# Performance work log

Hardware: AMD Instinct MI355X
Metric: run time of the kernel (lower is better)

The kernel has to match this reference:

```python
import jax, jax.numpy as jnp
import numpy as np

B, NI, H, NC = 524288, 32, 128, 64


def _masks(ni, h):
    deg_in = jnp.arange(ni)                     # input layer: arange % ni == arange
    deg_hid = jnp.arange(h) % (ni - 1)
    deg_out = jnp.arange(2 * ni) % ni - 1
    m1 = (deg_hid[:, None] >= deg_in[None, :]).astype(jnp.float32)   # [H, NI]
    m2 = (deg_hid[:, None] >= deg_hid[None, :]).astype(jnp.float32)  # [H, H]
    m3 = (deg_out[:, None] >= deg_hid[None, :]).astype(jnp.float32)  # [2NI, H]
    return m1, m2, m3


def setup_inputs() -> dict:
    key = jax.random.key(0)
    ks = jax.random.split(key, 9)
    s = 0.05
    return {
        "x": jax.random.normal(ks[0], (B, NI), jnp.float32),
        "cond": jax.random.normal(ks[1], (B, NC), jnp.float32),
        "W1": jax.random.normal(ks[2], (H, NI), jnp.float32) * s,
        "b1": jnp.zeros((H,), jnp.float32),
        "Wc": jax.random.normal(ks[3], (H, NC), jnp.float32) * s,
        "W2": jax.random.normal(ks[4], (H, H), jnp.float32) * s,
        "b2": jnp.zeros((H,), jnp.float32),
        "W3": jax.random.normal(ks[5], (2 * NI, H), jnp.float32) * s,
        "b3": jnp.zeros((2 * NI,), jnp.float32),
    }


def reference(x, cond, W1, b1, Wc, W2, b2, W3, b3):
    ni = x.shape[1]
    h_dim = W1.shape[0]
    m1, m2, m3 = _masks(ni, h_dim)
    # joiner: masked linear + conditioning linear (no bias on cond)
    h = x @ (W1 * m1).T + b1 + cond @ Wc.T            # [B, H]
    h = jax.nn.relu(h)
    h = jax.nn.relu(h @ (W2 * m2).T + b2)             # [B, H]
    o = h @ (W3 * m3).T + b3                          # [B, 2NI]
    m_, a = o[:, :ni], o[:, ni:]
    a = jnp.clip(a, -5.0, 5.0)
    u = (x - m_) * jnp.exp(-a)
    logdet = -jnp.sum(a, axis=-1, keepdims=True)
    return u, logdet
```

## Files before the change

### kernel.cpp

```cpp
#include <hip/hip_runtime.h>


#define B_ROWS 524288
#define NI 32
#define HD 128
#define NC 64

#define L2_BASE 24
#define L3_BASE 56
#define N_FRAGS 72

typedef _Float16 half8 __attribute__((ext_vector_type(8)));
typedef float f32x4 __attribute__((ext_vector_type(4)));

__device__ inline f32x4 relu4(f32x4 v) {
  v[0] = fmaxf(v[0], 0.f); v[1] = fmaxf(v[1], 0.f);
  v[2] = fmaxf(v[2], 0.f); v[3] = fmaxf(v[3], 0.f);
  return v;
}

__device__ inline half8 cvt8(f32x4 lo, f32x4 hi) {
  half8 h;
  h[0] = (_Float16)lo[0]; h[1] = (_Float16)lo[1];
  h[2] = (_Float16)lo[2]; h[3] = (_Float16)lo[3];
  h[4] = (_Float16)hi[0]; h[5] = (_Float16)hi[1];
  h[6] = (_Float16)hi[2]; h[7] = (_Float16)hi[3];
  return h;
}

__global__ void prep_weights(const float* __restrict__ W1, const float* __restrict__ Wc,
                             const float* __restrict__ W2, const float* __restrict__ W3,
                             _Float16* __restrict__ wf) {
  int tid = blockIdx.x * blockDim.x + threadIdx.x;
  if (tid >= N_FRAGS * 64) return;
  int frag = tid >> 6;
  int lane = tid & 63;
  int q = lane >> 4, c = lane & 15;
  int L, jt, kt;
  if (frag < L2_BASE)      { L = 0; jt = frag / 3;              kt = frag % 3; }
  else if (frag < L3_BASE) { L = 1; jt = (frag - L2_BASE) >> 2; kt = (frag - L2_BASE) & 3; }
  else                     { L = 2; jt = (frag - L3_BASE) >> 2; kt = (frag - L3_BASE) & 3; }
  int j = jt * 16 + c;
  half8 v;
#pragma unroll
  for (int e = 0; e < 8; ++e) {
    int k = kt * 32 + (e >> 2) * 16 + q * 4 + (e & 3);
    float w;
    if (L == 0) {
      if (k < NI) w = ((j % 31) >= k) ? W1[j * NI + k] : 0.f;
      else        w = Wc[j * NC + (k - NI)];
    } else if (L == 1) {
      w = ((j % 31) >= (k % 31)) ? W2[j * HD + k] : 0.f;
    } else {
      w = (((j % 32) - 1) >= (k % 31)) ? W3[j * HD + k] : 0.f;
    }
    v[e] = (_Float16)w;
  }
  *(half8*)(wf + (size_t)tid * 8) = v;
}

__global__ __launch_bounds__(512, 4) void made_fused(
    const float* __restrict__ x, const float* __restrict__ cond,
    const float* __restrict__ b1, const float* __restrict__ b2,
    const float* __restrict__ b3, const _Float16* __restrict__ wf,
    float* __restrict__ out) {
  __shared__ __align__(16) _Float16 wlds[48 * 512];

  const int tid  = threadIdx.x;
  const int lane = tid & 63;
  const int wid  = tid >> 6;
  const int q = lane >> 4, c = lane & 15;
  const long rowbase = ((long)blockIdx.x * 8 + wid) * 32;

  {
    const char* gsrc = (const char*)(wf + L2_BASE * 512) + wid * 6144;
    char* lbase = (char*)wlds + wid * 6144;
#pragma unroll
    for (int i = 0; i < 6; ++i) {
      __builtin_amdgcn_global_load_lds(
          (const __attribute__((address_space(1))) void*)(gsrc + i * 1024 + lane * 16),
          (__attribute__((address_space(3))) void*)(lbase + i * 1024),
          16, 0, 0);
    }
  }

  half8 bf[3][2];
#pragma unroll
  for (int nt = 0; nt < 2; ++nt) {
    const float* xr = x    + (rowbase + nt * 16 + c) * NI;
    const float* cr = cond + (rowbase + nt * 16 + c) * NC;
    bf[0][nt] = cvt8(*(const f32x4*)(xr + q * 4), *(const f32x4*)(xr + 16 + q * 4));
    bf[1][nt] = cvt8(*(const f32x4*)(cr + q * 4), *(const f32x4*)(cr + 16 + q * 4));
    bf[2][nt] = cvt8(*(const f32x4*)(cr + 32 + q * 4), *(const f32x4*)(cr + 48 + q * 4));
  }

  f32x4 acc[4][2];
  half8 h1[4][2];
#pragma unroll
  for (int jh = 0; jh < 2; ++jh) {
#pragma unroll
    for (int j4 = 0; j4 < 4; ++j4) {
      f32x4 bv = *(const f32x4*)(b1 + (jh * 4 + j4) * 16 + q * 4);
      acc[j4][0] = bv; acc[j4][1] = bv;
    }
#pragma unroll
    for (int j4 = 0; j4 < 4; ++j4) {
      int jt = jh * 4 + j4;
#pragma unroll
      for (int kt = 0; kt < 3; ++kt) {
        half8 a = *(const half8*)(wf + (((jt * 3 + kt) * 64 + lane) << 3));
#pragma unroll
        for (int nt = 0; nt < 2; ++nt)
          acc[j4][nt] = __builtin_amdgcn_mfma_f32_16x16x32_f16(a, bf[kt][nt], acc[j4][nt], 0, 0, 0);
      }
    }
#pragma unroll
    for (int p = 0; p < 2; ++p)
#pragma unroll
      for (int nt = 0; nt < 2; ++nt)
        h1[jh * 2 + p][nt] = cvt8(relu4(acc[p * 2][nt]), relu4(acc[p * 2 + 1][nt]));
  }

  __syncthreads();

  half8 h2[4][2];
#pragma unroll
  for (int jh = 0; jh < 2; ++jh) {
#pragma unroll
    for (int j4 = 0; j4 < 4; ++j4) {
      f32x4 bv = *(const f32x4*)(b2 + (jh * 4 + j4) * 16 + q * 4);
      acc[j4][0] = bv; acc[j4][1] = bv;
    }
#pragma unroll
    for (int j4 = 0; j4 < 4; ++j4) {
      int jt = jh * 4 + j4;
#pragma unroll
      for (int kt = 0; kt < 4; ++kt) {
        half8 a = *(const half8*)(wlds + (((jt * 4 + kt) * 64 + lane) << 3));
#pragma unroll
        for (int nt = 0; nt < 2; ++nt)
          acc[j4][nt] = __builtin_amdgcn_mfma_f32_16x16x32_f16(a, h1[kt][nt], acc[j4][nt], 0, 0, 0);
      }
    }
#pragma unroll
    for (int p = 0; p < 2; ++p)
#pragma unroll
      for (int nt = 0; nt < 2; ++nt)
        h2[jh * 2 + p][nt] = cvt8(relu4(acc[p * 2][nt]), relu4(acc[p * 2 + 1][nt]));
  }

#pragma unroll
  for (int jt = 0; jt < 4; ++jt) {
    f32x4 bv = *(const f32x4*)(b3 + jt * 16 + q * 4);
    acc[jt][0] = bv; acc[jt][1] = bv;
  }
#pragma unroll
  for (int jt = 0; jt < 4; ++jt)
#pragma unroll
    for (int kt = 0; kt < 4; ++kt) {
      half8 a = *(const half8*)(wlds + (((32 + jt * 4 + kt) * 64 + lane) << 3));
#pragma unroll
      for (int nt = 0; nt < 2; ++nt)
        acc[jt][nt] = __builtin_amdgcn_mfma_f32_16x16x32_f16(a, h2[kt][nt], acc[jt][nt], 0, 0, 0);
    }

#pragma unroll
  for (int nt = 0; nt < 2; ++nt) {
    long m = rowbase + nt * 16 + c;
    const float* xr = x + m * NI;
    f32x4 xa = *(const f32x4*)(xr + q * 4);
    f32x4 xb = *(const f32x4*)(xr + 16 + q * 4);
    f32x4 mva = acc[0][nt], mvb = acc[1][nt];
    f32x4 ava = acc[2][nt], avb = acc[3][nt];
    f32x4 ua, ub;
    float s = 0.f;
#pragma unroll
    for (int i = 0; i < 4; ++i) {
      float aa = fminf(fmaxf(ava[i], -5.f), 5.f);
      float ab = fminf(fmaxf(avb[i], -5.f), 5.f);
      ua[i] = (xa[i] - mva[i]) * __expf(-aa);
      ub[i] = (xb[i] - mvb[i]) * __expf(-ab);
      s += aa + ab;
    }
    *(f32x4*)(out + m * NI + q * 4) = ua;
    *(f32x4*)(out + m * NI + 16 + q * 4) = ub;
    s += __shfl_xor(s, 16);
    s += __shfl_xor(s, 32);
    if (q == 0) out[(long)B_ROWS * NI + m] = -s;
  }
}

extern "C" void kernel_launch(void* const* d_in, const int* in_sizes, int n_in,
                              void* d_out, int out_size, void* d_ws, size_t ws_size,
                              hipStream_t stream) {
  const float* x    = (const float*)d_in[0];
  const float* cond = (const float*)d_in[1];
  const float* W1   = (const float*)d_in[2];
  const float* b1   = (const float*)d_in[3];
  const float* Wc   = (const float*)d_in[4];
  const float* W2   = (const float*)d_in[5];
  const float* b2   = (const float*)d_in[6];
  const float* W3   = (const float*)d_in[7];
  const float* b3   = (const float*)d_in[8];
  _Float16* wf = (_Float16*)d_ws;

  prep_weights<<<(N_FRAGS * 64 + 255) / 256, 256, 0, stream>>>(W1, Wc, W2, W3, wf);
  made_fused<<<B_ROWS / 256, 512, 0, stream>>>(x, cond, b1, b2, b3, wf, (float*)d_out);
}
```

Before: 292.9 us.

## Make blocks persistent over row tiles with register double-buffered input prefetch

Each block now loops over four 128-row tiles, one 16-row tile per wave. The next tile's x and cond rows are prefetched into registers while the current tile runs its MFMAs. All three layers' weights and the biases are staged into LDS once per block, so the layer-1 weights are no longer read from global memory and the weight loads are spread over more rows. The trade-off is less MFMA work per wave per weight fetch (one 16-row N tile instead of two), more LDS, and fewer blocks in flight.

```diff
diff --git a/kernel.cpp b/kernel.cpp
--- a/kernel.cpp
+++ b/kernel.cpp
@@ -5,6 +5,7 @@
 #define NI 32
 #define HD 128
 #define NC 64
+#define ITERS 4
 
 #define L2_BASE 24
 #define L3_BASE 56
@@ -59,134 +60,139 @@
   *(half8*)(wf + (size_t)tid * 8) = v;
 }
 
+
+#define BODY(RX, RC, NRX, NRC, IT)                                            \
+  {                                                                           \
+    half8 bf0 = cvt8(RX[0], RX[1]);                                           \
+    half8 bf1 = cvt8(RC[0], RC[1]);                                           \
+    half8 bf2 = cvt8(RC[2], RC[3]);                                           \
+    if ((IT) < ITERS - 1) {     \
+      long nr = blockBase + ((IT) + 1) * 128 + wid * 16 + c;                  \
+      const f32x4* xr = (const f32x4*)(x + nr * NI);                          \
+      const f32x4* cr = (const f32x4*)(cond + nr * NC);                       \
+      NRX[0] = xr[q];     NRX[1] = xr[4 + q];                                 \
+      NRC[0] = cr[q];     NRC[1] = cr[4 + q];                                 \
+      NRC[2] = cr[8 + q]; NRC[3] = cr[12 + q];                                \
+    }                                                                         \
+    f32x4 acc[4]; half8 h1[4], h2[4];                                         \
+         \
+    _Pragma("unroll")                                                         \
+    for (int jh = 0; jh < 2; ++jh) {                                          \
+      _Pragma("unroll")                                                       \
+      for (int j4 = 0; j4 < 4; ++j4)                                          \
+        acc[j4] = *(const f32x4*)(blds + (jh * 4 + j4) * 16 + q * 4);         \
+      _Pragma("unroll")                                                       \
+      for (int j4 = 0; j4 < 4; ++j4) {                                        \
+        int jt = jh * 4 + j4;                                                 \
+        _Pragma("unroll")                                                     \
+        for (int kt = 0; kt < 3; ++kt) {                                      \
+          half8 a = *(const half8*)(wlds + (((jt * 3 + kt) * 64 + lane) << 3)); \
+          half8 bb = (kt == 0) ? bf0 : ((kt == 1) ? bf1 : bf2);               \
+          acc[j4] = __builtin_amdgcn_mfma_f32_16x16x32_f16(a, bb, acc[j4], 0, 0, 0); \
+        }                                                                     \
+      }                                                                       \
+      _Pragma("unroll")                                                       \
+      for (int p = 0; p < 2; ++p)                                             \
+        h1[jh * 2 + p] = cvt8(relu4(acc[p * 2]), relu4(acc[p * 2 + 1]));      \
+    }                                                                         \
+                                             \
+    _Pragma("unroll")                                                         \
+    for (int jh = 0; jh < 2; ++jh) {                                          \
+      _Pragma("unroll")                                                       \
+      for (int j4 = 0; j4 < 4; ++j4)                                          \
+        acc[j4] = *(const f32x4*)(blds + 128 + (jh * 4 + j4) * 16 + q * 4);   \
+      _Pragma("unroll")                                                       \
+      for (int j4 = 0; j4 < 4; ++j4) {                                        \
+        int jt = jh * 4 + j4;                                                 \
+        _Pragma("unroll")                                                     \
+        for (int kt = 0; kt < 4; ++kt) {                                      \
+          half8 a = *(const half8*)(wlds + (((L2_BASE + jt * 4 + kt) * 64 + lane) << 3)); \
+          acc[j4] = __builtin_amdgcn_mfma_f32_16x16x32_f16(a, h1[kt], acc[j4], 0, 0, 0); \
+        }                                                                     \
+      }                                                                       \
+      _Pragma("unroll")                                                       \
+      for (int p = 0; p < 2; ++p)                                             \
+        h2[jh * 2 + p] = cvt8(relu4(acc[p * 2]), relu4(acc[p * 2 + 1]));      \
+    }                                                                         \
+                \
+    _Pragma("unroll")                                                         \
+    for (int jt = 0; jt < 4; ++jt)                                            \
+      acc[jt] = *(const f32x4*)(blds + 256 + jt * 16 + q * 4);                \
+    _Pragma("unroll")                                                         \
+    for (int jt = 0; jt < 4; ++jt) {                                          \
+      _Pragma("unroll")                                                       \
+      for (int kt = 0; kt < 4; ++kt) {                                        \
+        half8 a = *(const half8*)(wlds + (((L3_BASE + jt * 4 + kt) * 64 + lane) << 3)); \
+        acc[jt] = __builtin_amdgcn_mfma_f32_16x16x32_f16(a, h2[kt], acc[jt], 0, 0, 0); \
+      }                                                                       \
+    }                                                                         \
+                      \
+    {                                                                         \
+      long m = blockBase + (IT) * 128 + wid * 16 + c;                         \
+      f32x4 xa = RX[0], xb = RX[1];                                           \
+      f32x4 ua, ub;                                                           \
+      float s = 0.f;                                                          \
+      _Pragma("unroll")                                                       \
+      for (int i = 0; i < 4; ++i) {                                           \
+        float aa = fminf(fmaxf(acc[2][i], -5.f), 5.f);                        \
+        float ab = fminf(fmaxf(acc[3][i], -5.f), 5.f);                        \
+        ua[i] = (xa[i] - acc[0][i]) * __expf(-aa);                            \
+        ub[i] = (xb[i] - acc[1][i]) * __expf(-ab);                            \
+        s += aa + ab;                                                         \
+      }                                                                       \
+      *(f32x4*)(out + m * NI + q * 4) = ua;                                   \
+      *(f32x4*)(out + m * NI + 16 + q * 4) = ub;                              \
+      s += __shfl_xor(s, 16);                                                 \
+      s += __shfl_xor(s, 32);                                                 \
+      if (q == 0) out[(long)B_ROWS * NI + m] = -s;                            \
+    }                                                                         \
+  }
+
 __global__ __launch_bounds__(512, 4) void made_fused(
     const float* __restrict__ x, const float* __restrict__ cond,
     const float* __restrict__ b1, const float* __restrict__ b2,
     const float* __restrict__ b3, const _Float16* __restrict__ wf,
     float* __restrict__ out) {
-  __shared__ __align__(16) _Float16 wlds[48 * 512];
+  __shared__ __align__(16) _Float16 wlds[N_FRAGS * 512];
+  __shared__ float blds[320];
 
   const int tid  = threadIdx.x;
   const int lane = tid & 63;
   const int wid  = tid >> 6;
   const int q = lane >> 4, c = lane & 15;
-  const long rowbase = ((long)blockIdx.x * 8 + wid) * 32;
+  const long blockBase = (long)blockIdx.x * (ITERS * 128);
 
   {
-    const char* gsrc = (const char*)(wf + L2_BASE * 512) + wid * 6144;
-    char* lbase = (char*)wlds + wid * 6144;
+    const char* gsrc = (const char*)wf + wid * 9216;
+    char* ldst = (char*)wlds + wid * 9216;
 #pragma unroll
-    for (int i = 0; i < 6; ++i) {
+    for (int i = 0; i < 9; ++i) {
       __builtin_amdgcn_global_load_lds(
           (const __attribute__((address_space(1))) void*)(gsrc + i * 1024 + lane * 16),
-          (__attribute__((address_space(3))) void*)(lbase + i * 1024),
+          (__attribute__((address_space(3))) void*)(ldst + i * 1024),
           16, 0, 0);
     }
   }
-
-  half8 bf[3][2];
-#pragma unroll
-  for (int nt = 0; nt < 2; ++nt) {
-    const float* xr = x    + (rowbase + nt * 16 + c) * NI;
-    const float* cr = cond + (rowbase + nt * 16 + c) * NC;
-    bf[0][nt] = cvt8(*(const f32x4*)(xr + q * 4), *(const f32x4*)(xr + 16 + q * 4));
-    bf[1][nt] = cvt8(*(const f32x4*)(cr + q * 4), *(const f32x4*)(cr + 16 + q * 4));
-    bf[2][nt] = cvt8(*(const f32x4*)(cr + 32 + q * 4), *(const f32x4*)(cr + 48 + q * 4));
-  }
-
-  f32x4 acc[4][2];
-  half8 h1[4][2];
-#pragma unroll
-  for (int jh = 0; jh < 2; ++jh) {
-#pragma unroll
-    for (int j4 = 0; j4 < 4; ++j4) {
-      f32x4 bv = *(const f32x4*)(b1 + (jh * 4 + j4) * 16 + q * 4);
-      acc[j4][0] = bv; acc[j4][1] = bv;
-    }
-#pragma unroll
-    for (int j4 = 0; j4 < 4; ++j4) {
-      int jt = jh * 4 + j4;
-#pragma unroll
-      for (int kt = 0; kt < 3; ++kt) {
-        half8 a = *(const half8*)(wf + (((jt * 3 + kt) * 64 + lane) << 3));
-#pragma unroll
-        for (int nt = 0; nt < 2; ++nt)
-          acc[j4][nt] = __builtin_amdgcn_mfma_f32_16x16x32_f16(a, bf[kt][nt], acc[j4][nt], 0, 0, 0);
-      }
-    }
-#pragma unroll
-    for (int p = 0; p < 2; ++p)
-#pragma unroll
-      for (int nt = 0; nt < 2; ++nt)
-        h1[jh * 2 + p][nt] = cvt8(relu4(acc[p * 2][nt]), relu4(acc[p * 2 + 1][nt]));
+  if (tid < 128)      blds[tid] = b1[tid];
+  else if (tid < 256) blds[tid] = b2[tid - 128];
+  else if (tid < 320) blds[tid] = b3[tid - 256];
+
+  f32x4 rxA[2], rcA[4], rxB[2], rcB[4];
+  {
+    long r = blockBase + wid * 16 + c;
+    const f32x4* xr = (const f32x4*)(x + r * NI);
+    const f32x4* cr = (const f32x4*)(cond + r * NC);
+    rxA[0] = xr[q];     rxA[1] = xr[4 + q];
+    rcA[0] = cr[q];     rcA[1] = cr[4 + q];
+    rcA[2] = cr[8 + q]; rcA[3] = cr[12 + q];
   }
 
   __syncthreads();
 
-  half8 h2[4][2];
-#pragma unroll
-  for (int jh = 0; jh < 2; ++jh) {
-#pragma unroll
-    for (int j4 = 0; j4 < 4; ++j4) {
-      f32x4 bv = *(const f32x4*)(b2 + (jh * 4 + j4) * 16 + q * 4);
-      acc[j4][0] = bv; acc[j4][1] = bv;
-    }
-#pragma unroll
-    for (int j4 = 0; j4 < 4; ++j4) {
-      int jt = jh * 4 + j4;
-#pragma unroll
-      for (int kt = 0; kt < 4; ++kt) {
-        half8 a = *(const half8*)(wlds + (((jt * 4 + kt) * 64 + lane) << 3));
-#pragma unroll
-        for (int nt = 0; nt < 2; ++nt)
-          acc[j4][nt] = __builtin_amdgcn_mfma_f32_16x16x32_f16(a, h1[kt][nt], acc[j4][nt], 0, 0, 0);
-      }
-    }
-#pragma unroll
-    for (int p = 0; p < 2; ++p)
-#pragma unroll
-      for (int nt = 0; nt < 2; ++nt)
-        h2[jh * 2 + p][nt] = cvt8(relu4(acc[p * 2][nt]), relu4(acc[p * 2 + 1][nt]));
-  }
-
-#pragma unroll
-  for (int jt = 0; jt < 4; ++jt) {
-    f32x4 bv = *(const f32x4*)(b3 + jt * 16 + q * 4);
-    acc[jt][0] = bv; acc[jt][1] = bv;
-  }
-#pragma unroll
-  for (int jt = 0; jt < 4; ++jt)
-#pragma unroll
-    for (int kt = 0; kt < 4; ++kt) {
-      half8 a = *(const half8*)(wlds + (((32 + jt * 4 + kt) * 64 + lane) << 3));
-#pragma unroll
-      for (int nt = 0; nt < 2; ++nt)
-        acc[jt][nt] = __builtin_amdgcn_mfma_f32_16x16x32_f16(a, h2[kt][nt], acc[jt][nt], 0, 0, 0);
-    }
-
-#pragma unroll
-  for (int nt = 0; nt < 2; ++nt) {
-    long m = rowbase + nt * 16 + c;
-    const float* xr = x + m * NI;
-    f32x4 xa = *(const f32x4*)(xr + q * 4);
-    f32x4 xb = *(const f32x4*)(xr + 16 + q * 4);
-    f32x4 mva = acc[0][nt], mvb = acc[1][nt];
-    f32x4 ava = acc[2][nt], avb = acc[3][nt];
-    f32x4 ua, ub;
-    float s = 0.f;
-#pragma unroll
-    for (int i = 0; i < 4; ++i) {
-      float aa = fminf(fmaxf(ava[i], -5.f), 5.f);
-      float ab = fminf(fmaxf(avb[i], -5.f), 5.f);
-      ua[i] = (xa[i] - mva[i]) * __expf(-aa);
-      ub[i] = (xb[i] - mvb[i]) * __expf(-ab);
-      s += aa + ab;
-    }
-    *(f32x4*)(out + m * NI + q * 4) = ua;
-    *(f32x4*)(out + m * NI + 16 + q * 4) = ub;
-    s += __shfl_xor(s, 16);
-    s += __shfl_xor(s, 32);
-    if (q == 0) out[(long)B_ROWS * NI + m] = -s;
+#pragma unroll 1
+  for (int ii = 0; ii < ITERS; ii += 2) {
+    BODY(rxA, rcA, rxB, rcB, ii);
+    BODY(rxB, rcB, rxA, rcA, ii + 1);
   }
 }
 
@@ -205,5 +211,5 @@
   _Float16* wf = (_Float16*)d_ws;
 
   prep_weights<<<(N_FRAGS * 64 + 255) / 256, 256, 0, stream>>>(W1, Wc, W2, W3, wf);
-  made_fused<<<B_ROWS / 256, 512, 0, stream>>>(x, cond, b1, b2, b3, wf, (float*)d_out);
-}
+  made_fused<<<B_ROWS / (ITERS * 128), 512, 0, stream>>>(x, cond, b1, b2, b3, wf, (float*)d_out);
+}
```

After: 1.042 ms. 256% more time.
